# Kernel tuning notes

Hardware: AMD Instinct MI355X
Metric: run time of the kernel (lower is better)

The kernel has to match this reference:

```python
import jax, jax.numpy as jnp
import numpy as np

N_NODES = 20000
N_EDGE_TYPES = 5
N_EDGES = 64000
IN_C, HID_C, OUT_C = 2048, 1024, 512


def setup_inputs() -> dict:
    key = jax.random.key(0)
    ks = jax.random.split(key, 12)
    s = 0.02
    return {
        "x": jax.random.normal(ks[0], (N_NODES, IN_C), jnp.float32),
        "edges": jax.random.randint(ks[1], (N_EDGE_TYPES, 2, N_EDGES), 0, N_NODES, dtype=jnp.int32),
        # SAGEConv weights, stacked over the 5 edge types. lin_l (neighbor agg, with bias), lin_r (root, no bias)
        "Wl1": jax.random.normal(ks[2], (N_EDGE_TYPES, HID_C, IN_C), jnp.float32) * s,
        "bl1": jnp.zeros((N_EDGE_TYPES, HID_C), jnp.float32),
        "Wr1": jax.random.normal(ks[3], (N_EDGE_TYPES, HID_C, IN_C), jnp.float32) * s,
        "Wl2": jax.random.normal(ks[4], (N_EDGE_TYPES, HID_C, HID_C), jnp.float32) * s,
        "bl2": jnp.zeros((N_EDGE_TYPES, HID_C), jnp.float32),
        "Wr2": jax.random.normal(ks[5], (N_EDGE_TYPES, HID_C, HID_C), jnp.float32) * s,
        "Wl3": jax.random.normal(ks[6], (N_EDGE_TYPES, OUT_C, HID_C), jnp.float32) * s,
        "bl3": jnp.zeros((N_EDGE_TYPES, OUT_C), jnp.float32),
        "Wr3": jax.random.normal(ks[7], (N_EDGE_TYPES, OUT_C, HID_C), jnp.float32) * s,
        "attn": jnp.ones((N_EDGE_TYPES,), jnp.float32),
    }


def sage_conv(h, src, dst, Wl, bl, Wr):
    # PyG SAGEConv(aggr='mean'): out = lin_l(mean_{j in N(i)} h_j) + lin_r(h_i)
    msg_sum = jax.ops.segment_sum(h[src], dst, num_segments=N_NODES)  # [N, C_in]
    deg = jax.ops.segment_sum(jnp.ones(src.shape, h.dtype), dst, num_segments=N_NODES)
    agg = msg_sum / jnp.maximum(deg, 1.0)[:, None]
    return agg @ Wl.T + bl + h @ Wr.T


def reference(x, edges, Wl1, bl1, Wr1, Wl2, bl2, Wr2, Wl3, bl3, Wr3, attn):
    outs = []
    for i in range(N_EDGE_TYPES):  # fixed small set of edge types
        src, dst = edges[i, 0], edges[i, 1]
        h = jax.nn.relu(sage_conv(x, src, dst, Wl1[i], bl1[i], Wr1[i]))
        h = jax.nn.relu(sage_conv(h, src, dst, Wl2[i], bl2[i], Wr2[i]))
        h = sage_conv(h, src, dst, Wl3[i], bl3[i], Wr3[i])  # no relu on final layer
        outs.append(h)
    w = jax.nn.softmax(attn)  # softmax-weighted combine over edge types
    combined = sum(w[i] * outs[i] for i in range(N_EDGE_TYPES))
    # F.normalize(p=2, dim=1, eps=1e-12)
    norm = jnp.linalg.norm(combined, axis=1, keepdims=True)
    return combined / jnp.maximum(norm, 1e-12)
```

## Files before the change

### kernel.cpp

```cpp
#include <hip/hip_runtime.h>
#include <hip/hip_bf16.h>
#include <stdint.h>

#define N_NODES   20000
#define MPAD      20224
#define N_TYPES   5
#define N_EDGES   64000
#define IN_C      2048
#define HID_C     1024
#define OUT_C     512

typedef __attribute__((ext_vector_type(8))) short short8;
typedef __attribute__((ext_vector_type(4))) float f32x4;

__device__ __forceinline__ unsigned short f2b(float f) {
  union { float f; uint32_t u; } c; c.f = f;
  uint32_t u = c.u;
  u += 0x7FFFu + ((u >> 16) & 1u);
  return (unsigned short)(u >> 16);
}
__device__ __forceinline__ float b2f(unsigned short h) {
  union { uint32_t u; float f; } c; c.u = ((uint32_t)h) << 16; return c.f;
}
__device__ __forceinline__ void gload_lds16(const void* g, void* l) {
  __builtin_amdgcn_global_load_lds((__attribute__((address_space(1))) void*)g,
                                   (__attribute__((address_space(3))) void*)l,
                                   16, 0, 0);
}

__global__ __launch_bounds__(64) void softmax5_k(const float* __restrict__ attn, float* __restrict__ w) {
  if (threadIdx.x == 0) {
    float m = attn[0];
    for (int i = 1; i < N_TYPES; ++i) m = fmaxf(m, attn[i]);
    float e[N_TYPES], s = 0.f;
    for (int i = 0; i < N_TYPES; ++i) { e[i] = expf(attn[i] - m); s += e[i]; }
    for (int i = 0; i < N_TYPES; ++i) w[i] = e[i] / s;
  }
}

__global__ __launch_bounds__(256) void zero_int_k(int* __restrict__ p, int n) {
  int i = blockIdx.x * 256 + threadIdx.x;
  if (i < n) p[i] = 0;
}

__global__ __launch_bounds__(256) void hist_k(const int* __restrict__ edges, int* __restrict__ deg) {
  int t = blockIdx.x * 256 + threadIdx.x;
  if (t < N_TYPES * N_EDGES) {
    int ty = t / N_EDGES, e = t - ty * N_EDGES;
    int dst = edges[ty * 2 * N_EDGES + N_EDGES + e];
    atomicAdd(&deg[ty * N_NODES + dst], 1);
  }
}

__global__ __launch_bounds__(256) void scan_k(const int* __restrict__ deg, int* __restrict__ rowptr,
                                              int* __restrict__ cursor) {
  int ty = blockIdx.x;
  const int* d = deg + ty * N_NODES;
  int* rp = rowptr + ty * (N_NODES + 1);
  int* cu = cursor + ty * N_NODES;
  __shared__ int sh[256];
  __shared__ int s_carry;
  int tid = threadIdx.x;
  if (tid == 0) s_carry = 0;
  __syncthreads();
  for (int base = 0; base < N_NODES; base += 256) {
    int i = base + tid;
    int v = (i < N_NODES) ? d[i] : 0;
    sh[tid] = v; __syncthreads();
    for (int off = 1; off < 256; off <<= 1) {
      int t2 = (tid >= off) ? sh[tid - off] : 0;
      __syncthreads();
      sh[tid] += t2;
      __syncthreads();
    }
    int incl = sh[tid];
    int c = s_carry;
    if (i < N_NODES) { rp[i] = c + incl - v; cu[i] = c + incl - v; }
    __syncthreads();
    if (tid == 255) s_carry = c + incl;
    __syncthreads();
  }
  if (tid == 0) rp[N_NODES] = s_carry;
}

__global__ __launch_bounds__(256) void scatter_k(const int* __restrict__ edges, int* __restrict__ cursor,
                                                 int* __restrict__ colidx) {
  int t = blockIdx.x * 256 + threadIdx.x;
  if (t < N_TYPES * N_EDGES) {
    int ty = t / N_EDGES, e = t - ty * N_EDGES;
    int src = edges[ty * 2 * N_EDGES + e];
    int dst = edges[ty * 2 * N_EDGES + N_EDGES + e];
    int pos = atomicAdd(&cursor[ty * N_NODES + dst], 1);
    colidx[ty * N_EDGES + pos] = src;
  }
}

__global__ __launch_bounds__(256) void cvt_x_k(const float* __restrict__ x, unsigned short* __restrict__ xb) {
  int i = blockIdx.x * 256 + threadIdx.x;
  int row = i >> 9;
  int c4 = (i & 511) << 2;
  if (row >= MPAD) return;
  ushort4 o;
  if (row < N_NODES) {
    float4 v = *(const float4*)(x + (size_t)row * IN_C + c4);
    o.x = f2b(v.x); o.y = f2b(v.y); o.z = f2b(v.z); o.w = f2b(v.w);
  } else { o.x = 0; o.y = 0; o.z = 0; o.w = 0; }
  *(ushort4*)(xb + (size_t)row * IN_C + c4) = o;
}

__global__ __launch_bounds__(256) void cvt_wcat_k(const float* __restrict__ s,
                                                  unsigned short* __restrict__ d,
                                                  int C, int K4, int rowoff) {
  int i = blockIdx.x * 256 + threadIdx.x;
  int total = N_TYPES * C * K4;
  if (i >= total) return;
  int k4 = i % K4;
  int rr = (i / K4) % C;
  int it = i / (C * K4);
  float4 v = ((const float4*)s)[i];
  ushort4 o; o.x = f2b(v.x); o.y = f2b(v.y); o.z = f2b(v.z); o.w = f2b(v.w);
  ((ushort4*)d)[((size_t)it * 2 * C + rowoff + rr) * K4 + k4] = o;
}

template<int NSIZE, int KSIZE>
__global__ __launch_bounds__(512, 2) void gemm_k(
    const unsigned short* __restrict__ Abase, size_t aS,
    const unsigned short* __restrict__ Wbase,
    unsigned short* __restrict__ PQ) {
  constexpr int NT = KSIZE / 32;
  constexpr int MT = MPAD / 256;
  constexpr int NB = NSIZE / 256;
  __shared__ unsigned short As[4][8192];
  __shared__ unsigned short Bs[4][8192];
  const int tid = threadIdx.x;
  const int lane = tid & 63;
  const int wave = tid >> 6;
  const int wm = wave >> 2, wn = wave & 3;

  const int nwg = gridDim.x;
  const int flat = blockIdx.x;
  const int q8 = nwg >> 3, r8 = nwg & 7;
  const int xcd = flat & 7, idx = flat >> 3;
  const int wg = (xcd < r8) ? (xcd * (q8 + 1) + idx) : (r8 * (q8 + 1) + (xcd - r8) * q8 + idx);
  const int itl = wg / (MT * NB);
  const int rem = wg % (MT * NB);
  const int row0 = (rem / NB) * 256;
  const int col0 = (rem % NB) * 256;

  const unsigned short* A = Abase + (size_t)itl * aS;
  const unsigned short* W = Wbase + (size_t)itl * NSIZE * KSIZE;

  const int sR = lane >> 3;
  const int su = (lane & 7) ^ (sR & 7);
  const int srow = 2 * sR + (su >> 2);
  const int selem = (su & 3) * 8;

  const int fr = lane & 15, k16 = lane >> 4;
  int aoff[8], boff[4];
#pragma unroll
  for (int m = 0; m < 8; ++m) {
    int r = wm * 128 + m * 16 + fr;
    aoff[m] = (((r >> 1) << 7) + ((r & 1) << 6) + (k16 << 4)) ^ (((r >> 1) & 7) << 4);
  }
#pragma unroll
  for (int n = 0; n < 4; ++n) {
    int r = wn * 64 + n * 16 + fr;
    boff[n] = (((r >> 1) << 7) + ((r & 1) << 6) + (k16 << 4)) ^ (((r >> 1) & 7) << 4);
  }

  auto stageA = [&](int t) {
    int s = t & 3; int kb = t * 32;
#pragma unroll
    for (int j = 0; j < 2; ++j) {
      int reg = wave + 8 * j;
      gload_lds16(A + (size_t)(row0 + reg * 16 + srow) * KSIZE + kb + selem, &As[s][reg * 512]);
    }
  };
  auto stageB = [&](int t) {
    int s = t & 3; int kb = t * 32;
#pragma unroll
    for (int j = 0; j < 2; ++j) {
      int reg = wave + 8 * j;
      gload_lds16(W + (size_t)(col0 + reg * 16 + srow) * KSIZE + kb + selem, &Bs[s][reg * 512]);
    }
  };

  f32x4 acc[8][4];
#pragma unroll
  for (int m = 0; m < 8; ++m)
#pragma unroll
    for (int n = 0; n < 4; ++n) acc[m][n] = (f32x4)(0.f);

  stageA(0); stageB(0);
  stageA(1); stageB(1);
  stageA(2); stageB(2);

  for (int t = 0; t < NT; ++t) {
    if (t < NT - 2)       asm volatile("s_waitcnt vmcnt(8)" ::: "memory");
    else if (t == NT - 2) asm volatile("s_waitcnt vmcnt(4)" ::: "memory");
    else                  asm volatile("s_waitcnt vmcnt(0)" ::: "memory");
    __builtin_amdgcn_s_barrier();
    __builtin_amdgcn_sched_barrier(0);
    const int slot = t & 3;
    const char* pa = (const char*)As[slot];
    const char* pb = (const char*)Bs[slot];
    short8 bf[4], af[8];
#pragma unroll
    for (int n = 0; n < 4; ++n) bf[n] = *(const short8*)(pb + boff[n]);
#pragma unroll
    for (int m = 0; m < 8; ++m) af[m] = *(const short8*)(pa + aoff[m]);
    if (t + 3 < NT) stageA(t + 3);
    __builtin_amdgcn_s_setprio(1);
#pragma unroll
    for (int m = 0; m < 4; ++m)
#pragma unroll
      for (int n = 0; n < 4; ++n)
        acc[m][n] = __builtin_amdgcn_mfma_f32_16x16x32_bf16(af[m], bf[n], acc[m][n], 0, 0, 0);
    __builtin_amdgcn_s_setprio(0);
    if (t + 3 < NT) stageB(t + 3);
    __builtin_amdgcn_s_setprio(1);
#pragma unroll
    for (int m = 0; m < 4; ++m)
#pragma unroll
      for (int n = 0; n < 4; ++n)
        acc[m + 4][n] = __builtin_amdgcn_mfma_f32_16x16x32_bf16(af[m + 4], bf[n], acc[m + 4][n], 0, 0, 0);
    __builtin_amdgcn_s_setprio(0);
  }

  const int erow = (lane >> 4) * 4;
  const int ecol = lane & 15;
  unsigned short* Op = PQ + (size_t)itl * MPAD * NSIZE;
#pragma unroll
  for (int m = 0; m < 8; ++m) {
#pragma unroll
    for (int n = 0; n < 4; ++n) {
      int gcol = col0 + wn * 64 + n * 16 + ecol;
#pragma unroll
      for (int r = 0; r < 4; ++r) {
        int grow = row0 + wm * 128 + m * 16 + erow + r;
        Op[(size_t)grow * NSIZE + gcol] = f2b(acc[m][n][r]);
      }
    }
  }
}

__global__ __launch_bounds__(256) void combine12_k(const unsigned short* __restrict__ PQ,
                                                   unsigned short* __restrict__ Hn,
                                                   const float* __restrict__ bl,
                                                   const int* __restrict__ rowptr,
                                                   const int* __restrict__ colidx, int it0) {
  constexpr int C = HID_C;
  int itl = blockIdx.x / MPAD;
  int node = blockIdx.x % MPAD;
  int it = it0 + itl;
  int tid = threadIdx.x;
  unsigned short* hp = Hn + ((size_t)itl * MPAD + node) * C + tid * 4;
  if (node >= N_NODES) {
    ushort4 z; z.x = 0; z.y = 0; z.z = 0; z.w = 0;
    *(ushort4*)hp = z;
    return;
  }
  const unsigned short* Pb = PQ + (size_t)itl * MPAD * 2 * C;
  const int* rp = rowptr + (size_t)it * (N_NODES + 1);
  const int* ci = colidx + (size_t)it * N_EDGES;
  int beg = rp[node], end = rp[node + 1];
  float a0 = 0.f, a1 = 0.f, a2 = 0.f, a3 = 0.f;
  for (int e = beg; e < end; ++e) {
    int src = ci[e];
    ushort4 u = *(const ushort4*)(Pb + (size_t)src * 2 * C + tid * 4);
    a0 += b2f(u.x); a1 += b2f(u.y); a2 += b2f(u.z); a3 += b2f(u.w);
  }
  float inv = (end > beg) ? 1.f / (float)(end - beg) : 0.f;
  a0 *= inv; a1 *= inv; a2 *= inv; a3 *= inv;
  ushort4 qv = *(const ushort4*)(Pb + (size_t)node * 2 * C + C + tid * 4);
  float4 bv = *(const float4*)(bl + (size_t)it * C + tid * 4);
  ushort4 o;
  o.x = f2b(fmaxf(a0 + b2f(qv.x) + bv.x, 0.f));
  o.y = f2b(fmaxf(a1 + b2f(qv.y) + bv.y, 0.f));
  o.z = f2b(fmaxf(a2 + b2f(qv.z) + bv.z, 0.f));
  o.w = f2b(fmaxf(a3 + b2f(qv.w) + bv.w, 0.f));
  *(ushort4*)hp = o;
}

__global__ __launch_bounds__(128) void combine3_k(const unsigned short* __restrict__ PQ,
                                                  const float* __restrict__ bl3,
                                                  const float* __restrict__ wsm,
                                                  const int* __restrict__ rowptr,
                                                  const int* __restrict__ colidx,
                                                  float* __restrict__ out, int it0, int nb, int acc) {
  int node = blockIdx.x;
  int tid = threadIdx.x;
  float s0 = 0.f, s1 = 0.f, s2 = 0.f, s3 = 0.f;
  for (int itl = 0; itl < nb; ++itl) {
    int it = it0 + itl;
    const unsigned short* Pb = PQ + (size_t)itl * MPAD * 1024;
    const int* rp = rowptr + (size_t)it * (N_NODES + 1);
    const int* ci = colidx + (size_t)it * N_EDGES;
    int beg = rp[node], end = rp[node + 1];
    float a0 = 0.f, a1 = 0.f, a2 = 0.f, a3 = 0.f;
    for (int e = beg; e < end; ++e) {
      int src = ci[e];
      ushort4 u = *(const ushort4*)(Pb + (size_t)src * 1024 + tid * 4);
      a0 += b2f(u.x); a1 += b2f(u.y); a2 += b2f(u.z); a3 += b2f(u.w);
    }
    float inv = (end > beg) ? 1.f / (float)(end - beg) : 0.f;
    ushort4 qv = *(const ushort4*)(Pb + (size_t)node * 1024 + 512 + tid * 4);
    float4 bv = *(const float4*)(bl3 + (size_t)it * OUT_C + tid * 4);
    float w = wsm[it];
    s0 += w * (a0 * inv + b2f(qv.x) + bv.x);
    s1 += w * (a1 * inv + b2f(qv.y) + bv.y);
    s2 += w * (a2 * inv + b2f(qv.z) + bv.z);
    s3 += w * (a3 * inv + b2f(qv.w) + bv.w);
  }
  float* op = out + (size_t)node * OUT_C + tid * 4;
  float4 cur = *(float4*)op;
  float4 nv;
  if (acc) { nv.x = cur.x + s0; nv.y = cur.y + s1; nv.z = cur.z + s2; nv.w = cur.w + s3; }
  else     { nv.x = s0; nv.y = s1; nv.z = s2; nv.w = s3; }
  *(float4*)op = nv;
}

__global__ __launch_bounds__(128) void l2norm_k(float* __restrict__ out) {
  int row = blockIdx.x;
  int tid = threadIdx.x;
  float4 v = ((float4*)(out + (size_t)row * OUT_C))[tid];
  float ss = v.x * v.x + v.y * v.y + v.z * v.z + v.w * v.w;
  for (int off = 32; off > 0; off >>= 1) ss += __shfl_down(ss, off);
  __shared__ float s2[2];
  if ((tid & 63) == 0) s2[tid >> 6] = ss;
  __syncthreads();
  float tot = s2[0] + s2[1];
  float inv = 1.f / fmaxf(sqrtf(tot), 1e-12f);
  v.x *= inv; v.y *= inv; v.z *= inv; v.w *= inv;
  ((float4*)(out + (size_t)row * OUT_C))[tid] = v;
}

extern "C" void kernel_launch(void* const* d_in, const int* in_sizes, int n_in,
                              void* d_out, int out_size, void* d_ws, size_t ws_size,
                              hipStream_t stream) {
  const float* x    = (const float*)d_in[0];
  const int*   edges = (const int*)d_in[1];
  const float* Wl1 = (const float*)d_in[2];
  const float* bl1 = (const float*)d_in[3];
  const float* Wr1 = (const float*)d_in[4];
  const float* Wl2 = (const float*)d_in[5];
  const float* bl2 = (const float*)d_in[6];
  const float* Wr2 = (const float*)d_in[7];
  const float* Wl3 = (const float*)d_in[8];
  const float* bl3 = (const float*)d_in[9];
  const float* Wr3 = (const float*)d_in[10];
  const float* attn = (const float*)d_in[11];
  float* out = (float*)d_out;

  char* ws = (char*)d_ws;
  size_t off = 0;
  auto alloc = [&](size_t bytes) -> char* {
    char* p = ws + off;
    off = (off + bytes + 255) & ~(size_t)255;
    return p;
  };
  float* wsm   = (float*)alloc(N_TYPES * 4);
  int* deg     = (int*)alloc((size_t)N_TYPES * N_NODES * 4);
  int* rowptr  = (int*)alloc((size_t)N_TYPES * (N_NODES + 1) * 4);
  int* cursor  = (int*)alloc((size_t)N_TYPES * N_NODES * 4);
  int* colidx  = (int*)alloc((size_t)N_TYPES * N_EDGES * 4);
  unsigned short* xb    = (unsigned short*)alloc((size_t)MPAD * IN_C * 2);
  unsigned short* wcat1 = (unsigned short*)alloc((size_t)N_TYPES * 2 * HID_C * IN_C * 2);
  unsigned short* wcat2 = (unsigned short*)alloc((size_t)N_TYPES * 2 * HID_C * HID_C * 2);
  unsigned short* wcat3 = (unsigned short*)alloc((size_t)N_TYPES * 2 * OUT_C * HID_C * 2);
  size_t persist = off;

  const size_t pqSlab = (size_t)MPAD * 2 * HID_C * 2;
  const size_t hSlab  = (size_t)MPAD * HID_C * 2;
  int nb = 1;
  for (int c = N_TYPES; c >= 1; --c) {
    size_t need = persist + (size_t)c * (pqSlab + hSlab) + 4096;
    if (need <= ws_size) { nb = c; break; }
  }
  unsigned short* PQ   = (unsigned short*)alloc((size_t)nb * pqSlab);
  unsigned short* hbuf = (unsigned short*)alloc((size_t)nb * hSlab);

  softmax5_k<<<1, 64, 0, stream>>>(attn, wsm);
  zero_int_k<<<(N_TYPES * N_NODES + 255) / 256, 256, 0, stream>>>(deg, N_TYPES * N_NODES);
  hist_k<<<(N_TYPES * N_EDGES + 255) / 256, 256, 0, stream>>>(edges, deg);
  scan_k<<<N_TYPES, 256, 0, stream>>>(deg, rowptr, cursor);
  scatter_k<<<(N_TYPES * N_EDGES + 255) / 256, 256, 0, stream>>>(edges, cursor, colidx);

  cvt_x_k<<<((size_t)MPAD * IN_C / 4 + 255) / 256, 256, 0, stream>>>(x, xb);
  {
    int t1 = N_TYPES * HID_C * (IN_C / 4);
    cvt_wcat_k<<<(t1 + 255) / 256, 256, 0, stream>>>(Wl1, wcat1, HID_C, IN_C / 4, 0);
    cvt_wcat_k<<<(t1 + 255) / 256, 256, 0, stream>>>(Wr1, wcat1, HID_C, IN_C / 4, HID_C);
    int t2 = N_TYPES * HID_C * (HID_C / 4);
    cvt_wcat_k<<<(t2 + 255) / 256, 256, 0, stream>>>(Wl2, wcat2, HID_C, HID_C / 4, 0);
    cvt_wcat_k<<<(t2 + 255) / 256, 256, 0, stream>>>(Wr2, wcat2, HID_C, HID_C / 4, HID_C);
    int t3 = N_TYPES * OUT_C * (HID_C / 4);
    cvt_wcat_k<<<(t3 + 255) / 256, 256, 0, stream>>>(Wl3, wcat3, OUT_C, HID_C / 4, 0);
    cvt_wcat_k<<<(t3 + 255) / 256, 256, 0, stream>>>(Wr3, wcat3, OUT_C, HID_C / 4, OUT_C);
  }

  const int MT = MPAD / 256;
  for (int g0 = 0; g0 < N_TYPES; g0 += nb) {
    int nbg = (N_TYPES - g0 < nb) ? (N_TYPES - g0) : nb;
    gemm_k<2 * HID_C, IN_C><<<nbg * MT * (2 * HID_C / 256), 512, 0, stream>>>(
        xb, 0, wcat1 + (size_t)g0 * 2 * HID_C * IN_C, PQ);
    combine12_k<<<nbg * MPAD, 256, 0, stream>>>(PQ, hbuf, bl1, rowptr, colidx, g0);
    gemm_k<2 * HID_C, HID_C><<<nbg * MT * (2 * HID_C / 256), 512, 0, stream>>>(
        hbuf, hSlab / 2, wcat2 + (size_t)g0 * 2 * HID_C * HID_C, PQ);
    combine12_k<<<nbg * MPAD, 256, 0, stream>>>(PQ, hbuf, bl2, rowptr, colidx, g0);
    gemm_k<2 * OUT_C, HID_C><<<nbg * MT * (2 * OUT_C / 256), 512, 0, stream>>>(
        hbuf, hSlab / 2, wcat3 + (size_t)g0 * 2 * OUT_C * HID_C, PQ);
    combine3_k<<<N_NODES, 128, 0, stream>>>(PQ, bl3, wsm, rowptr, colidx, out, g0, nbg,
                                            (g0 > 0) ? 1 : 0);
  }

  l2norm_k<<<N_NODES, 128, 0, stream>>>(out);
}
```

Baseline: 2.209 ms.

## Use double-buffered GEMM pipeline and fuse L2 norm into final combine

The GEMM shared-memory staging drops from a 4-slot, 3-deep prefetch ring to a 2-slot double buffer. This halves LDS use (64KB instead of 128KB per block), which may allow more blocks per CU, but only one k-tile of loads is now in flight and each iteration ends with a full vmcnt(0) wait plus a barrier. Separately, the final row L2 normalization moves into the last combine3 launch, removing one kernel launch and one read/write pass over the output.

```diff
diff --git a/kernel.cpp b/kernel.cpp
--- a/kernel.cpp
+++ b/kernel.cpp
@@ -130,8 +130,8 @@
   constexpr int NT = KSIZE / 32;
   constexpr int MT = MPAD / 256;
   constexpr int NB = NSIZE / 256;
-  __shared__ unsigned short As[4][8192];
-  __shared__ unsigned short Bs[4][8192];
+  __shared__ unsigned short As[2][8192];
+  __shared__ unsigned short Bs[2][8192];
   const int tid = threadIdx.x;
   const int lane = tid & 63;
   const int wave = tid >> 6;
@@ -169,7 +169,7 @@
   }
 
   auto stageA = [&](int t) {
-    int s = t & 3; int kb = t * 32;
+    int s = t & 1; int kb = t * 32;
 #pragma unroll
     for (int j = 0; j < 2; ++j) {
       int reg = wave + 8 * j;
@@ -177,7 +177,7 @@
     }
   };
   auto stageB = [&](int t) {
-    int s = t & 3; int kb = t * 32;
+    int s = t & 1; int kb = t * 32;
 #pragma unroll
     for (int j = 0; j < 2; ++j) {
       int reg = wave + 8 * j;
@@ -192,24 +192,20 @@
     for (int n = 0; n < 4; ++n) acc[m][n] = (f32x4)(0.f);
 
   stageA(0); stageB(0);
-  stageA(1); stageB(1);
-  stageA(2); stageB(2);
+  asm volatile("s_waitcnt vmcnt(0)" ::: "memory");
+  __builtin_amdgcn_s_barrier();
+  __builtin_amdgcn_sched_barrier(0);
 
   for (int t = 0; t < NT; ++t) {
-    if (t < NT - 2)       asm volatile("s_waitcnt vmcnt(8)" ::: "memory");
-    else if (t == NT - 2) asm volatile("s_waitcnt vmcnt(4)" ::: "memory");
-    else                  asm volatile("s_waitcnt vmcnt(0)" ::: "memory");
-    __builtin_amdgcn_s_barrier();
-    __builtin_amdgcn_sched_barrier(0);
-    const int slot = t & 3;
+    const int slot = t & 1;
     const char* pa = (const char*)As[slot];
     const char* pb = (const char*)Bs[slot];
+    if (t + 1 < NT) { stageA(t + 1); stageB(t + 1); }
     short8 bf[4], af[8];
 #pragma unroll
     for (int n = 0; n < 4; ++n) bf[n] = *(const short8*)(pb + boff[n]);
 #pragma unroll
     for (int m = 0; m < 8; ++m) af[m] = *(const short8*)(pa + aoff[m]);
-    if (t + 3 < NT) stageA(t + 3);
     __builtin_amdgcn_s_setprio(1);
 #pragma unroll
     for (int m = 0; m < 4; ++m)
@@ -217,7 +213,6 @@
       for (int n = 0; n < 4; ++n)
         acc[m][n] = __builtin_amdgcn_mfma_f32_16x16x32_bf16(af[m], bf[n], acc[m][n], 0, 0, 0);
     __builtin_amdgcn_s_setprio(0);
-    if (t + 3 < NT) stageB(t + 3);
     __builtin_amdgcn_s_setprio(1);
 #pragma unroll
     for (int m = 0; m < 4; ++m)
@@ -225,6 +220,9 @@
       for (int n = 0; n < 4; ++n)
         acc[m + 4][n] = __builtin_amdgcn_mfma_f32_16x16x32_bf16(af[m + 4], bf[n], acc[m + 4][n], 0, 0, 0);
     __builtin_amdgcn_s_setprio(0);
+    if (t + 1 < NT) asm volatile("s_waitcnt vmcnt(0)" ::: "memory");
+    __builtin_amdgcn_s_barrier();
+    __builtin_amdgcn_sched_barrier(0);
   }
 
   const int erow = (lane >> 4) * 4;
@@ -287,10 +285,12 @@
                                                   const float* __restrict__ wsm,
                                                   const int* __restrict__ rowptr,
                                                   const int* __restrict__ colidx,
-                                                  float* __restrict__ out, int it0, int nb, int acc) {
+                                                  float* __restrict__ out, int it0, int nb,
+                                                  int acc, int fin) {
+  __shared__ float s2[2];
   int node = blockIdx.x;
   int tid = threadIdx.x;
-  float s0 = 0.f, s1 = 0.f, s2 = 0.f, s3 = 0.f;
+  float s0 = 0.f, s1 = 0.f, s2v = 0.f, s3 = 0.f;
   for (int itl = 0; itl < nb; ++itl) {
     int it = it0 + itl;
     const unsigned short* Pb = PQ + (size_t)itl * MPAD * 1024;
@@ -309,30 +309,27 @@
     float w = wsm[it];
     s0 += w * (a0 * inv + b2f(qv.x) + bv.x);
     s1 += w * (a1 * inv + b2f(qv.y) + bv.y);
-    s2 += w * (a2 * inv + b2f(qv.z) + bv.z);
+    s2v += w * (a2 * inv + b2f(qv.z) + bv.z);
     s3 += w * (a3 * inv + b2f(qv.w) + bv.w);
   }
   float* op = out + (size_t)node * OUT_C + tid * 4;
-  float4 cur = *(float4*)op;
   float4 nv;
-  if (acc) { nv.x = cur.x + s0; nv.y = cur.y + s1; nv.z = cur.z + s2; nv.w = cur.w + s3; }
-  else     { nv.x = s0; nv.y = s1; nv.z = s2; nv.w = s3; }
+  if (acc) {
+    float4 cur = *(float4*)op;
+    nv.x = cur.x + s0; nv.y = cur.y + s1; nv.z = cur.z + s2v; nv.w = cur.w + s3;
+  } else {
+    nv.x = s0; nv.y = s1; nv.z = s2v; nv.w = s3;
+  }
+  if (fin) {
+    float ss = nv.x * nv.x + nv.y * nv.y + nv.z * nv.z + nv.w * nv.w;
+    for (int o2 = 32; o2 > 0; o2 >>= 1) ss += __shfl_down(ss, o2);
+    if ((tid & 63) == 0) s2[tid >> 6] = ss;
+    __syncthreads();
+    float tot = s2[0] + s2[1];
+    float inv = 1.f / fmaxf(sqrtf(tot), 1e-12f);
+    nv.x *= inv; nv.y *= inv; nv.z *= inv; nv.w *= inv;
+  }
   *(float4*)op = nv;
-}
-
-__global__ __launch_bounds__(128) void l2norm_k(float* __restrict__ out) {
-  int row = blockIdx.x;
-  int tid = threadIdx.x;
-  float4 v = ((float4*)(out + (size_t)row * OUT_C))[tid];
-  float ss = v.x * v.x + v.y * v.y + v.z * v.z + v.w * v.w;
-  for (int off = 32; off > 0; off >>= 1) ss += __shfl_down(ss, off);
-  __shared__ float s2[2];
-  if ((tid & 63) == 0) s2[tid >> 6] = ss;
-  __syncthreads();
-  float tot = s2[0] + s2[1];
-  float inv = 1.f / fmaxf(sqrtf(tot), 1e-12f);
-  v.x *= inv; v.y *= inv; v.z *= inv; v.w *= inv;
-  ((float4*)(out + (size_t)row * OUT_C))[tid] = v;
 }
 
 extern "C" void kernel_launch(void* const* d_in, const int* in_sizes, int n_in,
@@ -402,6 +399,7 @@
   const int MT = MPAD / 256;
   for (int g0 = 0; g0 < N_TYPES; g0 += nb) {
     int nbg = (N_TYPES - g0 < nb) ? (N_TYPES - g0) : nb;
+    int fin = (g0 + nbg >= N_TYPES) ? 1 : 0;
     gemm_k<2 * HID_C, IN_C><<<nbg * MT * (2 * HID_C / 256), 512, 0, stream>>>(
         xb, 0, wcat1 + (size_t)g0 * 2 * HID_C * IN_C, PQ);
     combine12_k<<<nbg * MPAD, 256, 0, stream>>>(PQ, hbuf, bl1, rowptr, colidx, g0);
@@ -411,8 +409,6 @@
     gemm_k<2 * OUT_C, HID_C><<<nbg * MT * (2 * OUT_C / 256), 512, 0, stream>>>(
         hbuf, hSlab / 2, wcat3 + (size_t)g0 * 2 * OUT_C * HID_C, PQ);
     combine3_k<<<N_NODES, 128, 0, stream>>>(PQ, bl3, wsm, rowptr, colidx, out, g0, nbg,
-                                            (g0 > 0) ? 1 : 0);
-  }
-
-  l2norm_k<<<N_NODES, 128, 0, stream>>>(out);
-}
+                                            (g0 > 0) ? 1 : 0, fin);
+  }
+}
```

Result: slower. 2.630 ms (+19.1%).
